# Kernel optimization log

Hardware: AMD Instinct MI355X
Metric: run time of the kernel (lower is better)

## Reference

```python
import jax, jax.numpy as jnp
import numpy as np

N = 50000
IN_DIM = 128
HID = 64
HEADS = 4
OUT_DIM = 2
NEG_SLOPE = 0.2


def setup_inputs() -> dict:
    key = jax.random.key(0)
    ks = jax.random.split(key, 10)
    x = jax.random.normal(ks[0], (N, IN_DIM), dtype=jnp.float32)
    edge_index = jax.random.randint(ks[1], (2, 800000), 0, N, dtype=jnp.int64)
    s = 0.1
    W1 = jax.random.normal(ks[2], (IN_DIM, HEADS * HID), dtype=jnp.float32) * s
    att_src1 = jax.random.normal(ks[3], (HEADS, HID), dtype=jnp.float32) * s
    att_dst1 = jax.random.normal(ks[4], (HEADS, HID), dtype=jnp.float32) * s
    b1 = jnp.zeros((HEADS * HID,), dtype=jnp.float32)
    W2 = jax.random.normal(ks[5], (HEADS * HID, 1 * OUT_DIM), dtype=jnp.float32) * s
    att_src2 = jax.random.normal(ks[6], (1, OUT_DIM), dtype=jnp.float32) * s
    att_dst2 = jax.random.normal(ks[7], (1, OUT_DIM), dtype=jnp.float32) * s
    b2 = jnp.zeros((OUT_DIM,), dtype=jnp.float32)
    return {"x": x, "edge_index": edge_index, "W1": W1, "att_src1": att_src1,
            "att_dst1": att_dst1, "b1": b1, "W2": W2, "att_src2": att_src2,
            "att_dst2": att_dst2, "b2": b2}


def gat_conv(x, W, att_src, att_dst, b, src, dst, heads, ch):
    # x: [N, F_in] -> h: [N, H, C]
    n = x.shape[0]
    h = (x @ W).reshape(n, heads, ch)
    a_s = jnp.einsum('nhc,hc->nh', h, att_src)  # [N, H]
    a_d = jnp.einsum('nhc,hc->nh', h, att_dst)  # [N, H]
    e = jax.nn.leaky_relu(a_s[src] + a_d[dst], NEG_SLOPE)  # [E, H]
    # segment softmax over incoming edges of each destination node
    m = jax.ops.segment_max(e, dst, num_segments=n)
    ex = jnp.exp(e - m[dst])
    z = jax.ops.segment_sum(ex, dst, num_segments=n)
    alpha = ex / z[dst]  # [E, H]
    msg = h[src] * alpha[:, :, None]  # [E, H, C]
    out = jax.ops.segment_sum(msg, dst, num_segments=n)  # [N, H, C]
    return out.reshape(n, heads * ch) + b


def reference(x, edge_index, W1, att_src1, att_dst1, b1, W2, att_src2, att_dst2, b2):
    n = x.shape[0]
    loop = jnp.arange(n, dtype=edge_index.dtype)
    src = jnp.concatenate([edge_index[0], loop])  # add_self_loops (PyG default)
    dst = jnp.concatenate([edge_index[1], loop])
    h = gat_conv(x, W1, att_src1, att_dst1, b1, src, dst, HEADS, HID)
    h = jax.nn.elu(h)
    # dropout is identity at inference
    out = gat_conv(h, W2, att_src2, att_dst2, b2, src, dst, 1, OUT_DIM)
    return out
```

## Files before the change

### kernel.cpp

```cpp
#include <hip/hip_runtime.h>

#define NN     50000
#define E_RAW  800000
#define ETOT   (E_RAW + NN)
#define FIN    128
#define FH     256
#define NEG    0.2f
#define BCAP   64

typedef __attribute__((ext_vector_type(8))) short s16x8;
typedef __attribute__((ext_vector_type(4))) float f32x4;

static __device__ __forceinline__ float leaky(float v) { return v > 0.f ? v : NEG * v; }

static __device__ __forceinline__ unsigned short f2bf(float f) {
    unsigned u = __float_as_uint(f);
    unsigned r = u + 0x7fffu + ((u >> 16) & 1u);
    return (unsigned short)(r >> 16);
}

__global__ __launch_bounds__(256) void k_prep(const float* __restrict__ W1,
                                              unsigned short* __restrict__ Wt_bf,
                                              int* __restrict__ cnt)
{
    const int b = blockIdx.x, t = threadIdx.x;
    if (b < FIN) Wt_bf[t * FIN + b] = f2bf(W1[b * FH + t]);
    int idx = b * 256 + t;
    if (idx < NN) cnt[idx] = 0;
}

__global__ __launch_bounds__(256) void k_gemm1(const float* __restrict__ x,
                                               const unsigned short* __restrict__ Wt_bf,
                                               const float* __restrict__ att_src,
                                               const float* __restrict__ att_dst,
                                               unsigned short* __restrict__ h1b,
                                               float* __restrict__ a_s,
                                               float* __restrict__ a_d)
{
    __shared__ unsigned short Wt[256][136];
    __shared__ unsigned short Xt[64][136];
    const int t    = threadIdx.x;
    const int w    = t >> 6;
    const int lane = t & 63;
    const int li   = lane & 15;
    const int q8   = (lane >> 4) * 8;
    const int quad = lane >> 4;
    const int n0   = blockIdx.x * 64;

#pragma unroll
    for (int i = 0; i < 16; i++) {
        int f = t + i * 256;
        int row = f >> 4, c16 = f & 15;
        *(uint4*)&Wt[row][c16 * 8] = *(const uint4*)&Wt_bf[row * FIN + c16 * 8];
    }
    {
        const int node_l = t >> 2;
        const int k0 = (t & 3) * 32;
        int nn = n0 + node_l; if (nn >= NN) nn = NN - 1;
        const float* xp = &x[(size_t)nn * FIN + k0];
        unsigned short* xd = &Xt[node_l][k0];
#pragma unroll
        for (int i = 0; i < 8; i++) {
            float4 v = *(const float4*)&xp[i * 4];
            xd[i * 4 + 0] = f2bf(v.x);
            xd[i * 4 + 1] = f2bf(v.y);
            xd[i * 4 + 2] = f2bf(v.z);
            xd[i * 4 + 3] = f2bf(v.w);
        }
    }
    __syncthreads();

    f32x4 acc[4][4];
#pragma unroll
    for (int i = 0; i < 4; i++)
#pragma unroll
        for (int j = 0; j < 4; j++) acc[i][j] = (f32x4){0.f, 0.f, 0.f, 0.f};

    for (int kk = 0; kk < FIN; kk += 32) {
        s16x8 af[4], bf[4];
#pragma unroll
        for (int m16 = 0; m16 < 4; m16++)
            af[m16] = *(const s16x8*)&Xt[m16 * 16 + li][kk + q8];
#pragma unroll
        for (int n16 = 0; n16 < 4; n16++)
            bf[n16] = *(const s16x8*)&Wt[w * 64 + n16 * 16 + li][kk + q8];
#pragma unroll
        for (int m16 = 0; m16 < 4; m16++)
#pragma unroll
            for (int n16 = 0; n16 < 4; n16++)
                acc[m16][n16] = __builtin_amdgcn_mfma_f32_16x16x32_bf16(
                    af[m16], bf[n16], acc[m16][n16], 0, 0, 0);
    }

    {
        float as_c[4], ad_c[4];
#pragma unroll
        for (int n16 = 0; n16 < 4; n16++) {
            int col = w * 64 + n16 * 16 + li;
            as_c[n16] = att_src[col];
            ad_c[n16] = att_dst[col];
        }
#pragma unroll
        for (int m16 = 0; m16 < 4; m16++) {
            float ps[4], pd[4];
#pragma unroll
            for (int reg = 0; reg < 4; reg++) {
                float s = 0.f, d = 0.f;
#pragma unroll
                for (int n16 = 0; n16 < 4; n16++) {
                    s += acc[m16][n16][reg] * as_c[n16];
                    d += acc[m16][n16][reg] * ad_c[n16];
                }
                ps[reg] = s; pd[reg] = d;
            }
#pragma unroll
            for (int off = 1; off < 16; off <<= 1) {
#pragma unroll
                for (int reg = 0; reg < 4; reg++) {
                    ps[reg] += __shfl_xor(ps[reg], off);
                    pd[reg] += __shfl_xor(pd[reg], off);
                }
            }
            if (li == 0) {
#pragma unroll
                for (int reg = 0; reg < 4; reg++) {
                    int node = n0 + m16 * 16 + quad * 4 + reg;
                    if (node < NN) {
                        a_s[node * 4 + w] = ps[reg];
                        a_d[node * 4 + w] = pd[reg];
                    }
                }
            }
        }
    }

    __syncthreads();
    unsigned short* Ot = &Wt[0][0];
#pragma unroll
    for (int m16 = 0; m16 < 4; m16++)
#pragma unroll
        for (int n16 = 0; n16 < 4; n16++)
#pragma unroll
            for (int reg = 0; reg < 4; reg++)
                Ot[(m16 * 16 + quad * 4 + reg) * FH + w * 64 + n16 * 16 + li] =
                    f2bf(acc[m16][n16][reg]);
    __syncthreads();
    {
        const int node_l = t >> 2;
        const int c0 = (t & 3) * 64;
        int node = n0 + node_l;
        if (node < NN) {
#pragma unroll
            for (int i = 0; i < 8; i++)
                *(uint4*)&h1b[(size_t)node * FH + c0 + i * 8] =
                    *(const uint4*)&Ot[node_l * FH + c0 + i * 8];
        }
    }
}

__global__ __launch_bounds__(256) void k_scatter(const int* __restrict__ ei,
                                                 int* __restrict__ cnt,
                                                 int* __restrict__ csr_src)
{
    const int e = blockIdx.x * 256 + threadIdx.x;
    if (e >= ETOT) return;
    int s, d;
    if (e < E_RAW) { s = ei[e]; d = ei[E_RAW + e]; } else { s = e - E_RAW; d = s; }
    int pos = atomicAdd(&cnt[d], 1);
    if (pos >= BCAP) return;
    csr_src[(d << 6) + pos] = s;
}

__global__ __launch_bounds__(256) void k_agg1(const int* __restrict__ cnt,
                                              const int* __restrict__ csr_src,
                                              const float* __restrict__ a_s1,
                                              const float* __restrict__ a_d1,
                                              const unsigned short* __restrict__ h1b,
                                              const float* __restrict__ b1,
                                              const float* __restrict__ W2,
                                              const float* __restrict__ att_src2,
                                              const float* __restrict__ att_dst2,
                                              float4* __restrict__ nd4)
{
    const int lane = threadIdx.x & 63;
    const int n = blockIdx.x * 4 + (threadIdx.x >> 6);
    if (n >= NN) return;
    int m = cnt[n]; if (m > BCAP) m = BCAP;
    const int base = n << 6;
    const int h = lane >> 4;
    const float ad_h = a_d1[n * 4 + h];
    float acc0 = 0.f, acc1 = 0.f, acc2 = 0.f, acc3 = 0.f, z = 0.f;
    const int* sp = &csr_src[base];
#pragma unroll 4
    for (int j = 0; j < m; j++) {
        int s = sp[j];
        float as_h = a_s1[s * 4 + h];
        float ex = __expf(leaky(as_h + ad_h));
        unsigned long long wv =
            *(const unsigned long long*)(h1b + (size_t)s * FH + lane * 4);
        unsigned lo = (unsigned)wv, hi = (unsigned)(wv >> 32);
        acc0 += __uint_as_float(lo << 16) * ex;
        acc1 += __uint_as_float(lo & 0xffff0000u) * ex;
        acc2 += __uint_as_float(hi << 16) * ex;
        acc3 += __uint_as_float(hi & 0xffff0000u) * ex;
        z += ex;
    }
    const int c0 = lane * 4;
    float4 bb = *(const float4*)&b1[c0];
    float v0 = acc0 / z + bb.x;
    float v1 = acc1 / z + bb.y;
    float v2 = acc2 / z + bb.z;
    float v3 = acc3 / z + bb.w;
    v0 = v0 > 0.f ? v0 : expm1f(v0);
    v1 = v1 > 0.f ? v1 : expm1f(v1);
    v2 = v2 > 0.f ? v2 : expm1f(v2);
    v3 = v3 > 0.f ? v3 : expm1f(v3);
    float4 w2a = *(const float4*)&W2[c0 * 2];
    float4 w2b = *(const float4*)&W2[c0 * 2 + 4];
    float s0 = v0 * w2a.x + v1 * w2a.z + v2 * w2b.x + v3 * w2b.z;
    float s1 = v0 * w2a.y + v1 * w2a.w + v2 * w2b.y + v3 * w2b.w;
#pragma unroll
    for (int off = 32; off; off >>= 1) {
        s0 += __shfl_xor(s0, off);
        s1 += __shfl_xor(s1, off);
    }
    if (lane == 0) {
        float4 nd;
        nd.x = s0; nd.y = s1;
        nd.z = s0 * att_src2[0] + s1 * att_src2[1];
        nd.w = s0 * att_dst2[0] + s1 * att_dst2[1];
        nd4[n] = nd;
    }
}

__global__ __launch_bounds__(256) void k_agg2(const int* __restrict__ cnt,
                                              const int* __restrict__ csr_src,
                                              const float4* __restrict__ nd4,
                                              const float* __restrict__ b2,
                                              float* __restrict__ out)
{
    const int l = threadIdx.x & 15;
    const int n = blockIdx.x * 16 + (threadIdx.x >> 4);
    if (n >= NN) return;
    int m = cnt[n]; if (m > BCAP) m = BCAP;
    const int base = n << 6;
    const float ad = nd4[n].w;
    float z = 0.f, a0 = 0.f, a1 = 0.f;
    for (int j = l; j < m; j += 16) {
        int s = csr_src[base + j];
        float4 f = nd4[s];
        float ex = __expf(leaky(f.z + ad));
        z  += ex;
        a0 += f.x * ex;
        a1 += f.y * ex;
    }
#pragma unroll
    for (int off = 8; off; off >>= 1) {
        z  += __shfl_xor(z, off);
        a0 += __shfl_xor(a0, off);
        a1 += __shfl_xor(a1, off);
    }
    if (l == 0) {
        out[n * 2 + 0] = a0 / z + b2[0];
        out[n * 2 + 1] = a1 / z + b2[1];
    }
}

extern "C" void kernel_launch(void* const* d_in, const int* in_sizes, int n_in,
                              void* d_out, int out_size, void* d_ws, size_t ws_size,
                              hipStream_t stream)
{
    const float* x        = (const float*)d_in[0];
    const int*   ei       = (const int*)d_in[1];
    const float* W1       = (const float*)d_in[2];
    const float* att_src1 = (const float*)d_in[3];
    const float* att_dst1 = (const float*)d_in[4];
    const float* b1       = (const float*)d_in[5];
    const float* W2       = (const float*)d_in[6];
    const float* att_src2 = (const float*)d_in[7];
    const float* att_dst2 = (const float*)d_in[8];
    const float* b2       = (const float*)d_in[9];
    float* out = (float*)d_out;

    int*    csr_src = (int*)d_ws;
    unsigned short* h1b = (unsigned short*)(csr_src + (size_t)NN * BCAP);
    unsigned short* Wt_bf = h1b + (size_t)NN * FH;
    int*    cnt   = (int*)(Wt_bf + FH * FIN);
    float*  a_s1  = (float*)(cnt + NN);
    float*  a_d1  = a_s1 + (size_t)NN * 4;
    float4* nd4   = (float4*)(a_d1 + (size_t)NN * 4);

    k_prep<<<200, 256, 0, stream>>>(W1, Wt_bf, cnt);
    k_gemm1<<<(NN + 63) / 64, 256, 0, stream>>>(x, Wt_bf, att_src1, att_dst1, h1b, a_s1, a_d1);
    k_scatter<<<(ETOT + 255) / 256, 256, 0, stream>>>(ei, cnt, csr_src);
    k_agg1<<<(NN + 3) / 4, 256, 0, stream>>>(cnt, csr_src, a_s1, a_d1, h1b,
                                             b1, W2, att_src2, att_dst2, nd4);
    k_agg2<<<(NN + 15) / 16, 256, 0, stream>>>(cnt, csr_src, nd4, b2, out);
}
```

Baseline: 243.2 us.

## Merge GEMM and edge-scatter kernels into one launch, read W from global

The GEMM kernel and the edge-scatter kernel now share one grid: the first blocks run the bf16 MFMA GEMM and the rest bucket edges by destination with atomics. This removes one launch and lets the two independent phases overlap on the GPU. The GEMM no longer stages W into LDS; B fragments are read straight from global/L2, which shrinks shared memory from about 87KB to 32KB for higher occupancy but adds repeated global loads. ELU's expm1f is swapped for __expf(v)-1, which loses some accuracy near zero.

```diff
diff --git a/kernel.cpp b/kernel.cpp
--- a/kernel.cpp
+++ b/kernel.cpp
@@ -7,6 +7,8 @@
 #define FH     256
 #define NEG    0.2f
 #define BCAP   64
+#define GEMM_NB ((NN + 63) / 64)
+#define SC_NB   ((ETOT + 255) / 256)
 
 typedef __attribute__((ext_vector_type(8))) short s16x8;
 typedef __attribute__((ext_vector_type(4))) float f32x4;
@@ -29,17 +31,31 @@
     if (idx < NN) cnt[idx] = 0;
 }
 
-__global__ __launch_bounds__(256) void k_gemm1(const float* __restrict__ x,
-                                               const unsigned short* __restrict__ Wt_bf,
-                                               const float* __restrict__ att_src,
-                                               const float* __restrict__ att_dst,
-                                               unsigned short* __restrict__ h1b,
-                                               float* __restrict__ a_s,
-                                               float* __restrict__ a_d)
-{
-    __shared__ unsigned short Wt[256][136];
-    __shared__ unsigned short Xt[64][136];
-    const int t    = threadIdx.x;
+__global__ __launch_bounds__(256) void k_gx(const float* __restrict__ x,
+                                            const unsigned short* __restrict__ Wt_bf,
+                                            const float* __restrict__ att_src,
+                                            const float* __restrict__ att_dst,
+                                            const int* __restrict__ ei,
+                                            int* __restrict__ cnt,
+                                            int* __restrict__ csr_src,
+                                            unsigned short* __restrict__ h1b,
+                                            float* __restrict__ a_s,
+                                            float* __restrict__ a_d)
+{
+    const int t = threadIdx.x;
+
+    if (blockIdx.x >= GEMM_NB) {
+        const int e = (blockIdx.x - GEMM_NB) * 256 + t;
+        if (e >= ETOT) return;
+        int s, d;
+        if (e < E_RAW) { s = ei[e]; d = ei[E_RAW + e]; } else { s = e - E_RAW; d = s; }
+        int pos = atomicAdd(&cnt[d], 1);
+        if (pos >= BCAP) return;
+        csr_src[(d << 6) + pos] = s;
+        return;
+    }
+
+    __shared__ unsigned short Sbuf[64 * 256];
     const int w    = t >> 6;
     const int lane = t & 63;
     const int li   = lane & 15;
@@ -47,18 +63,12 @@
     const int quad = lane >> 4;
     const int n0   = blockIdx.x * 64;
 
-#pragma unroll
-    for (int i = 0; i < 16; i++) {
-        int f = t + i * 256;
-        int row = f >> 4, c16 = f & 15;
-        *(uint4*)&Wt[row][c16 * 8] = *(const uint4*)&Wt_bf[row * FIN + c16 * 8];
-    }
     {
         const int node_l = t >> 2;
         const int k0 = (t & 3) * 32;
         int nn = n0 + node_l; if (nn >= NN) nn = NN - 1;
         const float* xp = &x[(size_t)nn * FIN + k0];
-        unsigned short* xd = &Xt[node_l][k0];
+        unsigned short* xd = &Sbuf[node_l * 136 + k0];
 #pragma unroll
         for (int i = 0; i < 8; i++) {
             float4 v = *(const float4*)&xp[i * 4];
@@ -76,14 +86,18 @@
 #pragma unroll
         for (int j = 0; j < 4; j++) acc[i][j] = (f32x4){0.f, 0.f, 0.f, 0.f};
 
-    for (int kk = 0; kk < FIN; kk += 32) {
+#pragma unroll
+    for (int kki = 0; kki < 4; kki++) {
+        const int kk = kki * 32;
         s16x8 af[4], bf[4];
 #pragma unroll
+        for (int n16 = 0; n16 < 4; n16++) {
+            int col = w * 64 + n16 * 16 + li;
+            bf[n16] = *(const s16x8*)&Wt_bf[col * FIN + kk + q8];
+        }
+#pragma unroll
         for (int m16 = 0; m16 < 4; m16++)
-            af[m16] = *(const s16x8*)&Xt[m16 * 16 + li][kk + q8];
-#pragma unroll
-        for (int n16 = 0; n16 < 4; n16++)
-            bf[n16] = *(const s16x8*)&Wt[w * 64 + n16 * 16 + li][kk + q8];
+            af[m16] = *(const s16x8*)&Sbuf[(m16 * 16 + li) * 136 + kk + q8];
 #pragma unroll
         for (int m16 = 0; m16 < 4; m16++)
 #pragma unroll
@@ -135,14 +149,13 @@
     }
 
     __syncthreads();
-    unsigned short* Ot = &Wt[0][0];
 #pragma unroll
     for (int m16 = 0; m16 < 4; m16++)
 #pragma unroll
         for (int n16 = 0; n16 < 4; n16++)
 #pragma unroll
             for (int reg = 0; reg < 4; reg++)
-                Ot[(m16 * 16 + quad * 4 + reg) * FH + w * 64 + n16 * 16 + li] =
+                Sbuf[(m16 * 16 + quad * 4 + reg) * FH + w * 64 + n16 * 16 + li] =
                     f2bf(acc[m16][n16][reg]);
     __syncthreads();
     {
@@ -153,22 +166,9 @@
 #pragma unroll
             for (int i = 0; i < 8; i++)
                 *(uint4*)&h1b[(size_t)node * FH + c0 + i * 8] =
-                    *(const uint4*)&Ot[node_l * FH + c0 + i * 8];
-        }
-    }
-}
-
-__global__ __launch_bounds__(256) void k_scatter(const int* __restrict__ ei,
-                                                 int* __restrict__ cnt,
-                                                 int* __restrict__ csr_src)
-{
-    const int e = blockIdx.x * 256 + threadIdx.x;
-    if (e >= ETOT) return;
-    int s, d;
-    if (e < E_RAW) { s = ei[e]; d = ei[E_RAW + e]; } else { s = e - E_RAW; d = s; }
-    int pos = atomicAdd(&cnt[d], 1);
-    if (pos >= BCAP) return;
-    csr_src[(d << 6) + pos] = s;
+                    *(const uint4*)&Sbuf[node_l * FH + c0 + i * 8];
+        }
+    }
 }
 
 __global__ __launch_bounds__(256) void k_agg1(const int* __restrict__ cnt,
@@ -211,10 +211,10 @@
     float v1 = acc1 / z + bb.y;
     float v2 = acc2 / z + bb.z;
     float v3 = acc3 / z + bb.w;
-    v0 = v0 > 0.f ? v0 : expm1f(v0);
-    v1 = v1 > 0.f ? v1 : expm1f(v1);
-    v2 = v2 > 0.f ? v2 : expm1f(v2);
-    v3 = v3 > 0.f ? v3 : expm1f(v3);
+    v0 = v0 > 0.f ? v0 : __expf(v0) - 1.f;
+    v1 = v1 > 0.f ? v1 : __expf(v1) - 1.f;
+    v2 = v2 > 0.f ? v2 : __expf(v2) - 1.f;
+    v3 = v3 > 0.f ? v3 : __expf(v3) - 1.f;
     float4 w2a = *(const float4*)&W2[c0 * 2];
     float4 w2b = *(const float4*)&W2[c0 * 2 + 4];
     float s0 = v0 * w2a.x + v1 * w2a.z + v2 * w2b.x + v3 * w2b.z;
@@ -291,8 +291,8 @@
     float4* nd4   = (float4*)(a_d1 + (size_t)NN * 4);
 
     k_prep<<<200, 256, 0, stream>>>(W1, Wt_bf, cnt);
-    k_gemm1<<<(NN + 63) / 64, 256, 0, stream>>>(x, Wt_bf, att_src1, att_dst1, h1b, a_s1, a_d1);
-    k_scatter<<<(ETOT + 255) / 256, 256, 0, stream>>>(ei, cnt, csr_src);
+    k_gx<<<GEMM_NB + SC_NB, 256, 0, stream>>>(x, Wt_bf, att_src1, att_dst1, ei,
+                                              cnt, csr_src, h1b, a_s1, a_d1);
     k_agg1<<<(NN + 3) / 4, 256, 0, stream>>>(cnt, csr_src, a_s1, a_d1, h1b,
                                              b1, W2, att_src2, att_dst2, nd4);
     k_agg2<<<(NN + 15) / 16, 256, 0, stream>>>(cnt, csr_src, nd4, b2, out);
```

Measured after the change: 233.3 us. 4.1% less time.
